# Performance work log

Hardware: AMD Instinct MI355X
Metric: run time of the kernel (lower is better)

Reference implementation:

```python
import jax, jax.numpy as jnp
import numpy as np

B, S, D, H = 2, 2048, 1024, 16
DK = D // H
EPS = 1e-6


def _rotate_half(x):
    x1, x2 = x[..., : x.shape[-1] // 2], x[..., x.shape[-1] // 2 :]
    return jnp.concatenate((-x2, x1), axis=-1)


def _rmsnorm(x, w):
    norm = jax.lax.rsqrt(jnp.mean(x * x, axis=-1, keepdims=True) + EPS)
    return x * norm * w


def setup_inputs() -> dict:
    key = jax.random.key(0)
    ks = jax.random.split(key, 12)
    q = jax.random.normal(ks[0], (B, S, D), jnp.float32)
    k = jax.random.normal(ks[1], (B, S, D), jnp.float32)
    v = jax.random.normal(ks[2], (B, S, D), jnp.float32)
    # causal mask, broadcastable over [B,H,S,S]; 0 => masked
    mask = jnp.tril(jnp.ones((S, S), jnp.int32))[None, None]
    # standard rotary tables
    inv_freq = 1.0 / (10000.0 ** (np.arange(0, DK, 2, dtype=np.float32) / DK))
    t = np.arange(S, dtype=np.float32)
    freqs = np.outer(t, inv_freq)  # [S, DK/2]
    emb = np.concatenate([freqs, freqs], axis=-1)  # [S, DK]
    cos = jnp.asarray(np.cos(emb))[None, None]  # [1,1,S,DK]
    sin = jnp.asarray(np.sin(emb))[None, None]
    sc = 1.0 / np.sqrt(D)
    wq = jax.random.normal(ks[3], (D, D), jnp.float32) * sc
    wk = jax.random.normal(ks[4], (D, D), jnp.float32) * sc
    wv = jax.random.normal(ks[5], (D, D), jnp.float32) * sc
    wo = jax.random.normal(ks[6], (D, D), jnp.float32) * sc
    bq = jnp.zeros((D,), jnp.float32)
    bk = jnp.zeros((D,), jnp.float32)
    bv = jnp.zeros((D,), jnp.float32)
    bo = jnp.zeros((D,), jnp.float32)
    qn_w = jnp.ones((DK,), jnp.float32)
    kn_w = jnp.ones((DK,), jnp.float32)
    return dict(q=q, k=k, v=v, mask=mask, cos=cos, sin=sin,
                wq=wq, bq=bq, wk=wk, bk=bk, wv=wv, bv=bv, wo=wo, bo=bo,
                qn_w=qn_w, kn_w=kn_w)


def reference(q, k, v, mask, cos, sin, wq, bq, wk, bk, wv, bv, wo, bo, qn_w, kn_w):
    b = q.shape[0]
    # QKV projections (torch Linear: x @ W.T + b)
    query = q @ wq.T + bq
    key = k @ wk.T + bk
    value = v @ wv.T + bv
    # [B,S,D] -> [B,H,S,DK]
    query = query.reshape(b, -1, H, DK).transpose(0, 2, 1, 3)
    key = key.reshape(b, -1, H, DK).transpose(0, 2, 1, 3)
    value = value.reshape(b, -1, H, DK).transpose(0, 2, 1, 3)
    # per-head QK RMSNorm
    query = _rmsnorm(query, qn_w)
    key = _rmsnorm(key, kn_w)
    # RoPE
    query = query * cos + _rotate_half(query) * sin
    key = key * cos + _rotate_half(key) * sin
    # naive attention
    scores = jnp.einsum('bhqd,bhkd->bhqk', query, key) / np.sqrt(DK).astype(np.float32)
    scores = jnp.where(mask == 0, jnp.float32(-1e9), scores)
    weights = jax.nn.softmax(scores, axis=-1)
    x = jnp.einsum('bhqk,bhkd->bhqd', weights, value)
    x = x.transpose(0, 2, 1, 3).reshape(b, -1, H * DK)
    return x @ wo.T + bo
```

## Files before the change

kernel.cpp:

```cpp
#include <hip/hip_runtime.h>

#define B_ 2
#define S_ 2048
#define D_ 1024
#define H_ 16
#define DK_ 64

typedef __attribute__((ext_vector_type(8))) short vshort8;
typedef __attribute__((ext_vector_type(4))) float vfloat4;

static __device__ inline unsigned short f2bf(float f) {
    unsigned int x = __float_as_uint(f);
    x += 0x7fffu + ((x >> 16) & 1u);
    return (unsigned short)(x >> 16);
}
static __device__ inline unsigned short f2bf_fast(float f) {
    return (unsigned short)((__float_as_uint(f) + 0x8000u) >> 16);
}
static __device__ inline float bf2f(unsigned short u) {
    return __uint_as_float((unsigned int)u << 16);
}

typedef __attribute__((address_space(1))) const unsigned int as1_uint;
typedef __attribute__((address_space(3))) unsigned int as3_uint;
static __device__ inline void async16(const void* g, void* l) {
    __builtin_amdgcn_global_load_lds((as1_uint*)g, (as3_uint*)l, 16, 0, 0);
}

__global__ __launch_bounds__(256) void cast_all_kernel(
    const float* __restrict__ q, const float* __restrict__ k, const float* __restrict__ v,
    const float* __restrict__ wq, const float* __restrict__ wk,
    const float* __restrict__ wv, const float* __restrict__ wo,
    unsigned short* __restrict__ xq, unsigned short* __restrict__ xk, unsigned short* __restrict__ xv,
    unsigned short* __restrict__ wqb, unsigned short* __restrict__ wkb,
    unsigned short* __restrict__ wvb, unsigned short* __restrict__ wob)
{
    long idx = ((long)blockIdx.x * 256 + threadIdx.x) * 8;
    int t22 = (int)(idx >> 22);
    const float* s;
    unsigned short* d;
    long off;
    if (t22 < 3) {
        s = (t22 == 0) ? q : (t22 == 1) ? k : v;
        d = (t22 == 0) ? xq : (t22 == 1) ? xk : xv;
        off = idx & ((1L << 22) - 1);
    } else {
        int w = (int)(idx >> 20) & 3;
        s = (w == 0) ? wq : (w == 1) ? wk : (w == 2) ? wv : wo;
        d = (w == 0) ? wqb : (w == 1) ? wkb : (w == 2) ? wvb : wob;
        off = idx & ((1L << 20) - 1);
    }
    float4 f0 = *(const float4*)(s + off);
    float4 f1 = *(const float4*)(s + off + 4);
    uint4 o;
    o.x = (unsigned int)f2bf(f0.x) | ((unsigned int)f2bf(f0.y) << 16);
    o.y = (unsigned int)f2bf(f0.z) | ((unsigned int)f2bf(f0.w) << 16);
    o.z = (unsigned int)f2bf(f1.x) | ((unsigned int)f2bf(f1.y) << 16);
    o.w = (unsigned int)f2bf(f1.z) | ((unsigned int)f2bf(f1.w) << 16);
    *(uint4*)(d + off) = o;
}

__global__ __launch_bounds__(256) void gemm_bt_kernel(
    const unsigned short* __restrict__ A0, const unsigned short* __restrict__ A1, const unsigned short* __restrict__ A2,
    const unsigned short* __restrict__ W0, const unsigned short* __restrict__ W1, const unsigned short* __restrict__ W2,
    const float* __restrict__ bb0, const float* __restrict__ bb1, const float* __restrict__ bb2,
    unsigned short* __restrict__ o0, unsigned short* __restrict__ o1, unsigned short* __restrict__ o2,
    float* __restrict__ of,
    const float* __restrict__ nw0, const float* __restrict__ nw1,
    const float* __restrict__ cosb, const float* __restrict__ sinb,
    int mode)
{
    __shared__ unsigned short As[2][128 * 32];
    __shared__ unsigned short Ws[2][128 * 32];

    const int z = blockIdx.z;
    const unsigned short* A    = (z == 0) ? A0 : (z == 1) ? A1 : A2;
    const unsigned short* Wt   = (z == 0) ? W0 : (z == 1) ? W1 : W2;
    const float* bias          = (z == 0) ? bb0 : (z == 1) ? bb1 : bb2;

    const int tid  = threadIdx.x;
    const int wave = tid >> 6;
    const int lane = tid & 63;
    const int l15  = lane & 15;
    const int quad = lane >> 4;
    const int wm   = wave >> 1;
    const int wn   = wave & 1;

    const int bid = blockIdx.y * 8 + blockIdx.x;
    const int byS = (bid & 7) * 4 + ((bid >> 3) & 3);
    const int bxS = bid >> 5;
    const int m0  = byS * 128;
    const int n0  = bxS * 128;

    const int li  = lane >> 2;
    const int lj  = lane & 3;
    const int lcc = (lj ^ ((li >> 1) & 3)) * 8;
    const int c0  = wave * 2;

    const unsigned short* gA0 = A  + (long)(m0 + c0 * 16      + li) * D_ + lcc;
    const unsigned short* gA1 = A  + (long)(m0 + c0 * 16 + 16 + li) * D_ + lcc;
    const unsigned short* gW0 = Wt + (long)(n0 + c0 * 16      + li) * D_ + lcc;
    const unsigned short* gW1 = Wt + (long)(n0 + c0 * 16 + 16 + li) * D_ + lcc;
    const int st0 = c0 * 512 + lane * 8;
    const int st1 = st0 + 512;

    vfloat4 acc[4][4];
    for (int rt = 0; rt < 4; rt++)
        for (int ct = 0; ct < 4; ct++) {
            vfloat4 zz = {0.f, 0.f, 0.f, 0.f};
            acc[rt][ct] = zz;
        }

    const int sw = (quad ^ ((l15 >> 1) & 3)) * 8;

    async16(gA0, &As[0][st0]);
    async16(gA1, &As[0][st1]);
    async16(gW0, &Ws[0][st0]);
    async16(gW1, &Ws[0][st1]);
    __syncthreads();

    for (int t = 0; t < 32; t++) {
        const int cur = t & 1;
        if (t < 31) {
            const int nxt = cur ^ 1;
            const int kn  = (t + 1) * 32;
            async16(gA0 + kn, &As[nxt][st0]);
            async16(gA1 + kn, &As[nxt][st1]);
            async16(gW0 + kn, &Ws[nxt][st0]);
            async16(gW1 + kn, &Ws[nxt][st1]);
        }

        vshort8 af[4], bf[4];
        for (int rt = 0; rt < 4; rt++)
            af[rt] = *(const vshort8*)&As[cur][(wm * 64 + rt * 16 + l15) * 32 + sw];
        for (int ct = 0; ct < 4; ct++)
            bf[ct] = *(const vshort8*)&Ws[cur][(wn * 64 + ct * 16 + l15) * 32 + sw];
        for (int rt = 0; rt < 4; rt++)
            for (int ct = 0; ct < 4; ct++)
                acc[rt][ct] = __builtin_amdgcn_mfma_f32_16x16x32_bf16(af[rt], bf[ct], acc[rt][ct], 0, 0, 0);

        __syncthreads();
    }

    if (mode == 0) {
        for (int rt = 0; rt < 4; rt++) {
            int row = m0 + wm * 64 + rt * 16 + quad * 4;
            for (int ct = 0; ct < 4; ct++) {
                int col = n0 + wn * 64 + ct * 16 + l15;
                float bvv = bias[col];
                for (int r = 0; r < 4; r++)
                    of[(long)(row + r) * D_ + col] = acc[rt][ct][r] + bvv;
            }
        }
    } else if (z == 2) {
        for (int rt = 0; rt < 4; rt++) {
            int row = m0 + wm * 64 + rt * 16 + quad * 4;
            for (int ct = 0; ct < 4; ct++) {
                int col = n0 + wn * 64 + ct * 16 + l15;
                float bvv = bias[col];
                for (int r = 0; r < 4; r++)
                    o2[(long)(row + r) * D_ + col] = f2bf(acc[rt][ct][r] + bvv);
            }
        }
    } else {
        const float* w      = (z == 0) ? nw0 : nw1;
        unsigned short* out = (z == 0) ? o0  : o1;
        const float sfac    = (z == 0) ? 0.18033688011112042f : 1.0f;
        const int h = bxS * 2 + wn;
        float wv4[4], bv4[4];
        for (int ct = 0; ct < 4; ct++) {
            int dk = ct * 16 + l15;
            wv4[ct] = w[dk];
            bv4[ct] = bias[n0 + wn * 64 + dk];
        }
        for (int rt = 0; rt < 4; rt++) {
            for (int r = 0; r < 4; r++) {
                int row = m0 + wm * 64 + rt * 16 + quad * 4 + r;
                int s = row & (S_ - 1);
                int b = row >> 11;
                float x0 = acc[rt][0][r] + bv4[0];
                float x1 = acc[rt][1][r] + bv4[1];
                float x2 = acc[rt][2][r] + bv4[2];
                float x3 = acc[rt][3][r] + bv4[3];
                float ss = (x0 * x0 + x1 * x1) + (x2 * x2 + x3 * x3);
                ss += __shfl_xor(ss, 1, 64);
                ss += __shfl_xor(ss, 2, 64);
                ss += __shfl_xor(ss, 4, 64);
                ss += __shfl_xor(ss, 8, 64);
                float rn = rsqrtf(ss * (1.0f / 64.0f) + 1e-6f);
                float n0v = x0 * rn * wv4[0];
                float n1v = x1 * rn * wv4[1];
                float n2v = x2 * rn * wv4[2];
                float n3v = x3 * rn * wv4[3];
                long csb = (long)s * DK_ + l15;
                float c0v = cosb[csb], c1v = cosb[csb + 16], c2v = cosb[csb + 32], c3v = cosb[csb + 48];
                float s0v = sinb[csb], s1v = sinb[csb + 16], s2v = sinb[csb + 32], s3v = sinb[csb + 48];
                float v0 = (n0v * c0v - n2v * s0v) * sfac;
                float v1 = (n1v * c1v - n3v * s1v) * sfac;
                float v2 = (n2v * c2v + n0v * s2v) * sfac;
                float v3 = (n3v * c3v + n1v * s3v) * sfac;
                long ob = ((long)(b * H_ + h) * S_ + s) * DK_ + l15;
                out[ob]      = f2bf(v0);
                out[ob + 16] = f2bf(v1);
                out[ob + 32] = f2bf(v2);
                out[ob + 48] = f2bf(v3);
            }
        }
    }
}

__global__ __launch_bounds__(256) void transpose_v_kernel(
    const unsigned short* __restrict__ X,
    unsigned short* __restrict__ Vt)
{
    __shared__ unsigned short T[64][72];
    int st = blockIdx.x, bh = blockIdx.y;
    int b = bh >> 4, h = bh & 15;
    int s0 = st * 64;

    for (int it = 0; it < 2; it++) {
        int idx = threadIdx.x + it * 256;
        int r = idx >> 3;
        int c = (idx & 7) * 8;
        *(uint4*)&T[r][c] = *(const uint4*)&X[(long)(b * S_ + s0 + r) * D_ + h * 64 + c];
    }
    __syncthreads();
    for (int it = 0; it < 2; it++) {
        int idx = threadIdx.x + it * 256;
        int dk = idx >> 3;
        int ss = (idx & 7) * 8;
        unsigned short pk[8];
        for (int j = 0; j < 8; j++) pk[j] = T[ss + j][dk];
        *(uint4*)&Vt[((long)(b * H_ + h) * DK_ + dk) * S_ + s0 + ss] = *(uint4*)pk;
    }
}

__global__ __launch_bounds__(256, 2) void attn_kernel(
    const unsigned short* __restrict__ Q,
    const unsigned short* __restrict__ K,
    const unsigned short* __restrict__ Vt,
    unsigned short* __restrict__ O)
{
    __shared__ unsigned short Kbuf[2][64 * 64];
    __shared__ unsigned short Vbuf[2][64 * 64];
    __shared__ unsigned short Pscr[4][2][16 * 72];

    const int tid  = threadIdx.x;
    const int wave = tid >> 6;
    const int lane = tid & 63;
    const int l15  = lane & 15;
    const int quad = lane >> 4;
    const int qa   = blockIdx.x;
    const int qb   = 31 - qa;
    const int bh   = blockIdx.y;
    const int b    = bh >> 4;
    const int h    = bh & 15;
    const long baseQ = (long)bh * S_ * DK_;
    const long baseV = (long)bh * DK_ * S_;
    const float FM = 13.0f;

    const int rowc  = lane >> 3;
    const int slotS = ((lane & 7) ^ rowc) * 8;
    const int cA    = wave * 2, cB = wave * 2 + 1;

    const unsigned short* gK0 = K  + baseQ + (long)(cA * 8 + rowc) * DK_ + slotS;
    const unsigned short* gK1 = K  + baseQ + (long)(cB * 8 + rowc) * DK_ + slotS;
    const unsigned short* gV0 = Vt + baseV + (long)(cA * 8 + rowc) * S_ + slotS;
    const unsigned short* gV1 = Vt + baseV + (long)(cB * 8 + rowc) * S_ + slotS;
    const int ldsOffA = cA * 512 + lane * 8;
    const int ldsOffB = cB * 512 + lane * 8;

    vshort8 bqA[2], bqB[2];
    {
        int qA = qa * 64 + wave * 16 + l15;
        int qB = qb * 64 + wave * 16 + l15;
        for (int kh = 0; kh < 2; kh++) {
            bqA[kh] = *(const vshort8*)&Q[baseQ + (long)qA * DK_ + kh * 32 + quad * 8];
            bqB[kh] = *(const vshort8*)&Q[baseQ + (long)qB * DK_ + kh * 32 + quad * 8];
        }
    }

    vfloat4 OaccA[4], OaccB[4];
    for (int dt = 0; dt < 4; dt++) {
        vfloat4 zz = {0.f, 0.f, 0.f, 0.f};
        OaccA[dt] = zz; OaccB[dt] = zz;
    }
    float rsA = 0.f, rsB = 0.f;

    unsigned short* PA = &Pscr[wave][0][0];
    unsigned short* PB = &Pscr[wave][1][0];

    const int nkt = qb + 1;

    async16(gK0, &Kbuf[0][ldsOffA]);
    async16(gK1, &Kbuf[0][ldsOffB]);
    async16(gV0, &Vbuf[0][ldsOffA]);
    async16(gV1, &Vbuf[0][ldsOffB]);
    __syncthreads();

    for (int t = 0; t < nkt; t++) {
        const int cur = t & 1;
        if (t + 1 < nkt) {
            const int nxt = cur ^ 1;
            const long ko = (long)(t + 1) * 64;
            async16(gK0 + ko * DK_, &Kbuf[nxt][ldsOffA]);
            async16(gK1 + ko * DK_, &Kbuf[nxt][ldsOffB]);
            async16(gV0 + ko,       &Vbuf[nxt][ldsOffA]);
            async16(gV1 + ko,       &Vbuf[nxt][ldsOffB]);
        }

        vshort8 ak[4][2];
        for (int ct = 0; ct < 4; ct++)
            for (int kh = 0; kh < 2; kh++) {
                int r = ct * 16 + l15;
                int sl = (kh * 4 + quad) ^ (l15 & 7);
                ak[ct][kh] = *(const vshort8*)&Kbuf[cur][r * 64 + sl * 8];
            }
        vshort8 av[4][2];
        for (int dt = 0; dt < 4; dt++)
            for (int kh = 0; kh < 2; kh++) {
                int r = dt * 16 + l15;
                int sl = (kh * 4 + quad) ^ (l15 & 7);
                av[dt][kh] = *(const vshort8*)&Vbuf[cur][r * 64 + sl * 8];
            }

        const int k0 = t * 64;
        const bool actA = (t <= qa);

        if (actA) {
            vfloat4 sc[4];
            for (int ct = 0; ct < 4; ct++) {
                vfloat4 a = {0.f, 0.f, 0.f, 0.f};
                a = __builtin_amdgcn_mfma_f32_16x16x32_bf16(ak[ct][0], bqA[0], a, 0, 0, 0);
                a = __builtin_amdgcn_mfma_f32_16x16x32_bf16(ak[ct][1], bqA[1], a, 0, 0, 0);
                sc[ct] = a;
            }
            if (t == qa) {
                int qg = qa * 64 + wave * 16 + l15;
                for (int ct = 0; ct < 4; ct++) {
                    int kvb = k0 + ct * 16 + quad * 4;
                    for (int r = 0; r < 4; r++)
                        if (kvb + r > qg) sc[ct][r] = -1e30f;
                }
            }
            for (int ct = 0; ct < 4; ct++) {
                float p0 = exp2f(sc[ct][0] - FM);
                float p1 = exp2f(sc[ct][1] - FM);
                float p2 = exp2f(sc[ct][2] - FM);
                float p3 = exp2f(sc[ct][3] - FM);
                rsA += (p0 + p1) + (p2 + p3);
                uint2 o;
                o.x = (unsigned int)f2bf_fast(p0) | ((unsigned int)f2bf_fast(p1) << 16);
                o.y = (unsigned int)f2bf_fast(p2) | ((unsigned int)f2bf_fast(p3) << 16);
                *(uint2*)&PA[l15 * 72 + ct * 16 + quad * 4] = o;
            }
            vshort8 bp[2];
            for (int kh = 0; kh < 2; kh++)
                bp[kh] = *(const vshort8*)&PA[l15 * 72 + kh * 32 + quad * 8];
            for (int dt = 0; dt < 4; dt++) {
                OaccA[dt] = __builtin_amdgcn_mfma_f32_16x16x32_bf16(av[dt][0], bp[0], OaccA[dt], 0, 0, 0);
                OaccA[dt] = __builtin_amdgcn_mfma_f32_16x16x32_bf16(av[dt][1], bp[1], OaccA[dt], 0, 0, 0);
            }
        }

        {
            vfloat4 sc[4];
            for (int ct = 0; ct < 4; ct++) {
                vfloat4 a = {0.f, 0.f, 0.f, 0.f};
                a = __builtin_amdgcn_mfma_f32_16x16x32_bf16(ak[ct][0], bqB[0], a, 0, 0, 0);
                a = __builtin_amdgcn_mfma_f32_16x16x32_bf16(ak[ct][1], bqB[1], a, 0, 0, 0);
                sc[ct] = a;
            }
            if (t == nkt - 1) {
                int qg = qb * 64 + wave * 16 + l15;
                for (int ct = 0; ct < 4; ct++) {
                    int kvb = k0 + ct * 16 + quad * 4;
                    for (int r = 0; r < 4; r++)
                        if (kvb + r > qg) sc[ct][r] = -1e30f;
                }
            }
            for (int ct = 0; ct < 4; ct++) {
                float p0 = exp2f(sc[ct][0] - FM);
                float p1 = exp2f(sc[ct][1] - FM);
                float p2 = exp2f(sc[ct][2] - FM);
                float p3 = exp2f(sc[ct][3] - FM);
                rsB += (p0 + p1) + (p2 + p3);
                uint2 o;
                o.x = (unsigned int)f2bf_fast(p0) | ((unsigned int)f2bf_fast(p1) << 16);
                o.y = (unsigned int)f2bf_fast(p2) | ((unsigned int)f2bf_fast(p3) << 16);
                *(uint2*)&PB[l15 * 72 + ct * 16 + quad * 4] = o;
            }
            vshort8 bp[2];
            for (int kh = 0; kh < 2; kh++)
                bp[kh] = *(const vshort8*)&PB[l15 * 72 + kh * 32 + quad * 8];
            for (int dt = 0; dt < 4; dt++) {
                OaccB[dt] = __builtin_amdgcn_mfma_f32_16x16x32_bf16(av[dt][0], bp[0], OaccB[dt], 0, 0, 0);
                OaccB[dt] = __builtin_amdgcn_mfma_f32_16x16x32_bf16(av[dt][1], bp[1], OaccB[dt], 0, 0, 0);
            }
        }

        __syncthreads();
    }

    rsA += __shfl_xor(rsA, 16, 64);
    rsA += __shfl_xor(rsA, 32, 64);
    rsB += __shfl_xor(rsB, 16, 64);
    rsB += __shfl_xor(rsB, 32, 64);

    {
        float inv = 1.0f / rsA;
        int qg = qa * 64 + wave * 16 + l15;
        long rowbase = (long)(b * S_ + qg) * D_ + h * 64;
        for (int dt = 0; dt < 4; dt++) {
            unsigned short pk[4];
            for (int r = 0; r < 4; r++) pk[r] = f2bf(OaccA[dt][r] * inv);
            uint2 o;
            o.x = (unsigned int)pk[0] | ((unsigned int)pk[1] << 16);
            o.y = (unsigned int)pk[2] | ((unsigned int)pk[3] << 16);
            *(uint2*)&O[rowbase + dt * 16 + quad * 4] = o;
        }
    }
    {
        float inv = 1.0f / rsB;
        int qg = qb * 64 + wave * 16 + l15;
        long rowbase = (long)(b * S_ + qg) * D_ + h * 64;
        for (int dt = 0; dt < 4; dt++) {
            unsigned short pk[4];
            for (int r = 0; r < 4; r++) pk[r] = f2bf(OaccB[dt][r] * inv);
            uint2 o;
            o.x = (unsigned int)pk[0] | ((unsigned int)pk[1] << 16);
            o.y = (unsigned int)pk[2] | ((unsigned int)pk[3] << 16);
            *(uint2*)&O[rowbase + dt * 16 + quad * 4] = o;
        }
    }
}

extern "C" void kernel_launch(void* const* d_in, const int* in_sizes, int n_in,
                              void* d_out, int out_size, void* d_ws, size_t ws_size,
                              hipStream_t stream) {
    const float* q    = (const float*)d_in[0];
    const float* k    = (const float*)d_in[1];
    const float* v    = (const float*)d_in[2];
    const float* cosb = (const float*)d_in[4];
    const float* sinb = (const float*)d_in[5];
    const float* wq   = (const float*)d_in[6];
    const float* bq   = (const float*)d_in[7];
    const float* wk   = (const float*)d_in[8];
    const float* bk   = (const float*)d_in[9];
    const float* wv   = (const float*)d_in[10];
    const float* bv   = (const float*)d_in[11];
    const float* wo   = (const float*)d_in[12];
    const float* bo   = (const float*)d_in[13];
    const float* qn_w = (const float*)d_in[14];
    const float* kn_w = (const float*)d_in[15];

    const long MB = 1024 * 1024;
    char* ws = (char*)d_ws;
    unsigned short* xq   = (unsigned short*)(ws + 0 * MB);
    unsigned short* xk   = (unsigned short*)(ws + 8 * MB);
    unsigned short* xv   = (unsigned short*)(ws + 16 * MB);
    unsigned short* wqb  = (unsigned short*)(ws + 24 * MB);
    unsigned short* wkb  = (unsigned short*)(ws + 26 * MB);
    unsigned short* wvb  = (unsigned short*)(ws + 28 * MB);
    unsigned short* wob  = (unsigned short*)(ws + 30 * MB);
    unsigned short* Qn   = (unsigned short*)(ws + 32 * MB);
    unsigned short* Kn   = (unsigned short*)(ws + 40 * MB);
    unsigned short* tmpv = (unsigned short*)(ws + 48 * MB);
    unsigned short* Vtb  = (unsigned short*)(ws + 56 * MB);
    unsigned short* Ob   = (unsigned short*)(ws + 64 * MB);

    dim3 blk(256);
    cast_all_kernel<<<dim3(8192), blk, 0, stream>>>(
        q, k, v, wq, wk, wv, wo, xq, xk, xv, wqb, wkb, wvb, wob);

    gemm_bt_kernel<<<dim3(8, 32, 3), blk, 0, stream>>>(
        xq, xk, xv, wqb, wkb, wvb, bq, bk, bv,
        Qn, Kn, tmpv, nullptr, qn_w, kn_w, cosb, sinb, 1);

    transpose_v_kernel<<<dim3(32, 32), blk, 0, stream>>>(tmpv, Vtb);

    attn_kernel<<<dim3(16, 32), blk, 0, stream>>>(Qn, Kn, Vtb, Ob);

    gemm_bt_kernel<<<dim3(8, 32, 1), blk, 0, stream>>>(
        Ob, Ob, Ob, wob, wob, wob, bo, bo, bo,
        nullptr, nullptr, nullptr, (float*)d_out, nullptr, nullptr, nullptr, nullptr, 0);
}
```

Before: 272.1 us.

## Fuse V transpose into QKV GEMM epilogue and shrink GEMM tile to 128x64

The GEMM tile goes from 128x128 to 128x64, with each wave now owning a 32x64 slice, so each block covers exactly one head's columns. The grid doubles, and launch bounds now request higher occupancy. The V projection epilogue stages its bf16 output transposed in shared memory and writes the head-major V^T layout directly, which removes the separate transpose kernel and its global round trip. In exchange, operand reuse per block drops: A tiles are reloaded twice as often, and each MFMA step does less work per LDS load.

```diff
diff --git a/kernel.cpp b/kernel.cpp
--- a/kernel.cpp
+++ b/kernel.cpp
@@ -60,7 +60,7 @@
     *(uint4*)(d + off) = o;
 }
 
-__global__ __launch_bounds__(256) void gemm_bt_kernel(
+__global__ __launch_bounds__(256, 5) void gemm_bt_kernel(
     const unsigned short* __restrict__ A0, const unsigned short* __restrict__ A1, const unsigned short* __restrict__ A2,
     const unsigned short* __restrict__ W0, const unsigned short* __restrict__ W1, const unsigned short* __restrict__ W2,
     const float* __restrict__ bb0, const float* __restrict__ bb1, const float* __restrict__ bb2,
@@ -70,8 +70,7 @@
     const float* __restrict__ cosb, const float* __restrict__ sinb,
     int mode)
 {
-    __shared__ unsigned short As[2][128 * 32];
-    __shared__ unsigned short Ws[2][128 * 32];
+    __shared__ __align__(16) unsigned char smem[2][12288];
 
     const int z = blockIdx.z;
     const unsigned short* A    = (z == 0) ? A0 : (z == 1) ? A1 : A2;
@@ -83,29 +82,26 @@
     const int lane = tid & 63;
     const int l15  = lane & 15;
     const int quad = lane >> 4;
-    const int wm   = wave >> 1;
-    const int wn   = wave & 1;
-
-    const int bid = blockIdx.y * 8 + blockIdx.x;
+
+    const int bid = blockIdx.y * 16 + blockIdx.x;
     const int byS = (bid & 7) * 4 + ((bid >> 3) & 3);
     const int bxS = bid >> 5;
     const int m0  = byS * 128;
-    const int n0  = bxS * 128;
+    const int n0  = bxS * 64;
 
     const int li  = lane >> 2;
     const int lj  = lane & 3;
     const int lcc = (lj ^ ((li >> 1) & 3)) * 8;
-    const int c0  = wave * 2;
-
-    const unsigned short* gA0 = A  + (long)(m0 + c0 * 16      + li) * D_ + lcc;
-    const unsigned short* gA1 = A  + (long)(m0 + c0 * 16 + 16 + li) * D_ + lcc;
-    const unsigned short* gW0 = Wt + (long)(n0 + c0 * 16      + li) * D_ + lcc;
-    const unsigned short* gW1 = Wt + (long)(n0 + c0 * 16 + 16 + li) * D_ + lcc;
-    const int st0 = c0 * 512 + lane * 8;
-    const int st1 = st0 + 512;
-
-    vfloat4 acc[4][4];
-    for (int rt = 0; rt < 4; rt++)
+
+    const unsigned short* gA0 = A  + (long)(m0 + wave * 32      + li) * D_ + lcc;
+    const unsigned short* gA1 = A  + (long)(m0 + wave * 32 + 16 + li) * D_ + lcc;
+    const unsigned short* gW0 = Wt + (long)(n0 + wave * 16      + li) * D_ + lcc;
+    const int stA0 = wave * 1024 + lane * 8;
+    const int stA1 = stA0 + 512;
+    const int stW  = wave * 512 + lane * 8;
+
+    vfloat4 acc[2][4];
+    for (int rt = 0; rt < 2; rt++)
         for (int ct = 0; ct < 4; ct++) {
             vfloat4 zz = {0.f, 0.f, 0.f, 0.f};
             acc[rt][ct] = zz;
@@ -113,29 +109,35 @@
 
     const int sw = (quad ^ ((l15 >> 1) & 3)) * 8;
 
-    async16(gA0, &As[0][st0]);
-    async16(gA1, &As[0][st1]);
-    async16(gW0, &Ws[0][st0]);
-    async16(gW1, &Ws[0][st1]);
+    unsigned short* As0 = (unsigned short*)&smem[0][0];
+    unsigned short* As1 = (unsigned short*)&smem[1][0];
+    unsigned short* Ws0 = (unsigned short*)&smem[0][8192];
+    unsigned short* Ws1 = (unsigned short*)&smem[1][8192];
+
+    async16(gA0, As0 + stA0);
+    async16(gA1, As0 + stA1);
+    async16(gW0, Ws0 + stW);
     __syncthreads();
 
     for (int t = 0; t < 32; t++) {
         const int cur = t & 1;
+        unsigned short* Asc = cur ? As1 : As0;
+        unsigned short* Wsc = cur ? Ws1 : Ws0;
         if (t < 31) {
-            const int nxt = cur ^ 1;
-            const int kn  = (t + 1) * 32;
-            async16(gA0 + kn, &As[nxt][st0]);
-            async16(gA1 + kn, &As[nxt][st1]);
-            async16(gW0 + kn, &Ws[nxt][st0]);
-            async16(gW1 + kn, &Ws[nxt][st1]);
-        }
-
-        vshort8 af[4], bf[4];
-        for (int rt = 0; rt < 4; rt++)
-            af[rt] = *(const vshort8*)&As[cur][(wm * 64 + rt * 16 + l15) * 32 + sw];
+            unsigned short* Asn = cur ? As0 : As1;
+            unsigned short* Wsn = cur ? Ws0 : Ws1;
+            const int kn = (t + 1) * 32;
+            async16(gA0 + kn, Asn + stA0);
+            async16(gA1 + kn, Asn + stA1);
+            async16(gW0 + kn, Wsn + stW);
+        }
+
+        vshort8 af[2], bf[4];
+        for (int rt = 0; rt < 2; rt++)
+            af[rt] = *(const vshort8*)&Asc[(wave * 32 + rt * 16 + l15) * 32 + sw];
         for (int ct = 0; ct < 4; ct++)
-            bf[ct] = *(const vshort8*)&Ws[cur][(wn * 64 + ct * 16 + l15) * 32 + sw];
-        for (int rt = 0; rt < 4; rt++)
+            bf[ct] = *(const vshort8*)&Wsc[(ct * 16 + l15) * 32 + sw];
+        for (int rt = 0; rt < 2; rt++)
             for (int ct = 0; ct < 4; ct++)
                 acc[rt][ct] = __builtin_amdgcn_mfma_f32_16x16x32_bf16(af[rt], bf[ct], acc[rt][ct], 0, 0, 0);
 
@@ -143,39 +145,53 @@
     }
 
     if (mode == 0) {
-        for (int rt = 0; rt < 4; rt++) {
-            int row = m0 + wm * 64 + rt * 16 + quad * 4;
-            for (int ct = 0; ct < 4; ct++) {
-                int col = n0 + wn * 64 + ct * 16 + l15;
+        for (int rt = 0; rt < 2; rt++) {
+            int row = m0 + wave * 32 + rt * 16 + quad * 4;
+            for (int ct = 0; ct < 4; ct++) {
+                int col = n0 + ct * 16 + l15;
                 float bvv = bias[col];
                 for (int r = 0; r < 4; r++)
                     of[(long)(row + r) * D_ + col] = acc[rt][ct][r] + bvv;
             }
         }
     } else if (z == 2) {
-        for (int rt = 0; rt < 4; rt++) {
-            int row = m0 + wm * 64 + rt * 16 + quad * 4;
-            for (int ct = 0; ct < 4; ct++) {
-                int col = n0 + wn * 64 + ct * 16 + l15;
-                float bvv = bias[col];
-                for (int r = 0; r < 4; r++)
-                    o2[(long)(row + r) * D_ + col] = f2bf(acc[rt][ct][r] + bvv);
-            }
-        }
+        unsigned short* T = (unsigned short*)&smem[0][0];
+        float bv4[4];
+        for (int ct = 0; ct < 4; ct++) bv4[ct] = bias[n0 + ct * 16 + l15];
+        for (int rt = 0; rt < 2; rt++) {
+            int sl0 = wave * 32 + rt * 16 + quad * 4;
+            for (int ct = 0; ct < 4; ct++) {
+                unsigned short pk[4];
+                for (int r = 0; r < 4; r++) pk[r] = f2bf(acc[rt][ct][r] + bv4[ct]);
+                uint2 o;
+                o.x = (unsigned int)pk[0] | ((unsigned int)pk[1] << 16);
+                o.y = (unsigned int)pk[2] | ((unsigned int)pk[3] << 16);
+                *(uint2*)&T[(ct * 16 + l15) * 136 + sl0] = o;
+            }
+        }
+        __syncthreads();
+        const int dk = tid >> 2;
+        const int sc = (tid & 3) * 32;
+        const int b  = byS >> 4;
+        const int s0 = (byS & 15) * 128;
+        const unsigned short* src = &T[dk * 136 + sc];
+        unsigned short* dst = o2 + (((long)(b * H_ + bxS) * DK_ + dk) * S_) + s0 + sc;
+        for (int j = 0; j < 4; j++)
+            *(uint4*)(dst + j * 8) = *(const uint4*)(src + j * 8);
     } else {
         const float* w      = (z == 0) ? nw0 : nw1;
         unsigned short* out = (z == 0) ? o0  : o1;
         const float sfac    = (z == 0) ? 0.18033688011112042f : 1.0f;
-        const int h = bxS * 2 + wn;
+        const int h = bxS;
         float wv4[4], bv4[4];
         for (int ct = 0; ct < 4; ct++) {
             int dk = ct * 16 + l15;
             wv4[ct] = w[dk];
-            bv4[ct] = bias[n0 + wn * 64 + dk];
-        }
-        for (int rt = 0; rt < 4; rt++) {
+            bv4[ct] = bias[n0 + dk];
+        }
+        for (int rt = 0; rt < 2; rt++) {
             for (int r = 0; r < 4; r++) {
-                int row = m0 + wm * 64 + rt * 16 + quad * 4 + r;
+                int row = m0 + wave * 32 + rt * 16 + quad * 4 + r;
                 int s = row & (S_ - 1);
                 int b = row >> 11;
                 float x0 = acc[rt][0][r] + bv4[0];
@@ -209,32 +225,6 @@
     }
 }
 
-__global__ __launch_bounds__(256) void transpose_v_kernel(
-    const unsigned short* __restrict__ X,
-    unsigned short* __restrict__ Vt)
-{
-    __shared__ unsigned short T[64][72];
-    int st = blockIdx.x, bh = blockIdx.y;
-    int b = bh >> 4, h = bh & 15;
-    int s0 = st * 64;
-
-    for (int it = 0; it < 2; it++) {
-        int idx = threadIdx.x + it * 256;
-        int r = idx >> 3;
-        int c = (idx & 7) * 8;
-        *(uint4*)&T[r][c] = *(const uint4*)&X[(long)(b * S_ + s0 + r) * D_ + h * 64 + c];
-    }
-    __syncthreads();
-    for (int it = 0; it < 2; it++) {
-        int idx = threadIdx.x + it * 256;
-        int dk = idx >> 3;
-        int ss = (idx & 7) * 8;
-        unsigned short pk[8];
-        for (int j = 0; j < 8; j++) pk[j] = T[ss + j][dk];
-        *(uint4*)&Vt[((long)(b * H_ + h) * DK_ + dk) * S_ + s0 + ss] = *(uint4*)pk;
-    }
-}
-
 __global__ __launch_bounds__(256, 2) void attn_kernel(
     const unsigned short* __restrict__ Q,
     const unsigned short* __restrict__ K,
@@ -465,7 +455,6 @@
     unsigned short* wob  = (unsigned short*)(ws + 30 * MB);
     unsigned short* Qn   = (unsigned short*)(ws + 32 * MB);
     unsigned short* Kn   = (unsigned short*)(ws + 40 * MB);
-    unsigned short* tmpv = (unsigned short*)(ws + 48 * MB);
     unsigned short* Vtb  = (unsigned short*)(ws + 56 * MB);
     unsigned short* Ob   = (unsigned short*)(ws + 64 * MB);
 
@@ -473,15 +462,13 @@
     cast_all_kernel<<<dim3(8192), blk, 0, stream>>>(
         q, k, v, wq, wk, wv, wo, xq, xk, xv, wqb, wkb, wvb, wob);
 
-    gemm_bt_kernel<<<dim3(8, 32, 3), blk, 0, stream>>>(
+    gemm_bt_kernel<<<dim3(16, 32, 3), blk, 0, stream>>>(
         xq, xk, xv, wqb, wkb, wvb, bq, bk, bv,
-        Qn, Kn, tmpv, nullptr, qn_w, kn_w, cosb, sinb, 1);
-
-    transpose_v_kernel<<<dim3(32, 32), blk, 0, stream>>>(tmpv, Vtb);
+        Qn, Kn, Vtb, nullptr, qn_w, kn_w, cosb, sinb, 1);
 
     attn_kernel<<<dim3(16, 32), blk, 0, stream>>>(Qn, Kn, Vtb, Ob);
 
-    gemm_bt_kernel<<<dim3(8, 32, 1), blk, 0, stream>>>(
+    gemm_bt_kernel<<<dim3(16, 32, 1), blk, 0, stream>>>(
         Ob, Ob, Ob, wob, wob, wob, bo, bo, bo,
         nullptr, nullptr, nullptr, (float*)d_out, nullptr, nullptr, nullptr, nullptr, 0);
 }
```

New measurement: 242.6 us. 1.12x faster.
